# Performance work log

Hardware: AMD Instinct MI355X
Metric: run time of the kernel (lower is better)

Reference implementation:

```python
import jax, jax.numpy as jnp
import numpy as np

D_MODEL = 1024
D_FFN = 4096
NUM_EXPERTS = 8
TOP_K = 2
EPS = 1e-7


def setup_inputs() -> dict:
    key = jax.random.key(0)
    ks = jax.random.split(key, 10)
    B, T = 2, 2048
    s = 0.02
    return {
        "x": jax.random.normal(ks[0], (B, T, D_MODEL), dtype=jnp.float32),
        "padding_mask": jnp.ones((B, T), dtype=bool),
        "rms_w": jnp.ones((D_MODEL,), dtype=jnp.float32),
        "router_w": jax.random.normal(ks[1], (NUM_EXPERTS, D_MODEL), dtype=jnp.float32) * s,
        "router_b": jnp.zeros((NUM_EXPERTS,), dtype=jnp.float32),
        "W1": jax.random.normal(ks[2], (NUM_EXPERTS, D_MODEL, D_FFN), dtype=jnp.float32) * s,
        "b1": jnp.zeros((NUM_EXPERTS, D_FFN), dtype=jnp.float32),
        "W2": jax.random.normal(ks[3], (NUM_EXPERTS, D_FFN, D_MODEL), dtype=jnp.float32) * s,
        "b2": jnp.zeros((NUM_EXPERTS, D_MODEL), dtype=jnp.float32),
        "W3": jax.random.normal(ks[4], (NUM_EXPERTS, D_MODEL, D_FFN), dtype=jnp.float32) * s,
        "b3": jnp.zeros((NUM_EXPERTS, D_FFN), dtype=jnp.float32),
    }


def reference(x, padding_mask, rms_w, router_w, router_b, W1, b1, W2, b2, W3, b3):
    B, T, d = x.shape
    # RMSNorm
    rms = jnp.sqrt(jnp.mean(x * x, axis=-1, keepdims=True) + EPS)
    xn = rms_w * (x / rms)
    xf = xn.reshape(-1, d)  # [N, d]

    # Router: softmax -> top-k -> renormalize
    logits = xf @ router_w.T + router_b            # [N, E]
    probs = jax.nn.softmax(logits, axis=-1)
    topv, topi = jax.lax.top_k(probs, TOP_K)       # [N, K]
    w = topv / jnp.sum(topv, axis=-1, keepdims=True)
    # Dense combine weights per (token, expert): sum of top-k weights routed to e
    combine = jnp.sum(jax.nn.one_hot(topi, NUM_EXPERTS, dtype=xf.dtype) * w[..., None], axis=1)  # [N, E]

    # Loop over experts via scan (one full-token SwiGLU FFN per expert, masked combine)
    def step(acc, params):
        W1e, b1e, W2e, b2e, W3e, b3e, ce = params
        h = jax.nn.silu(xf @ W1e + b1e) * (xf @ W3e + b3e)  # [N, d_ffn]
        y = h @ W2e + b2e                                    # [N, d]
        return acc + ce[:, None] * y, None

    out, _ = jax.lax.scan(step, jnp.zeros_like(xf), (W1, b1, W2, b2, W3, b3, combine.T))
    aux_loss = jnp.asarray(0.0, dtype=x.dtype)  # use_aux_loss only active in training mode
    return out.reshape(B, T, d), aux_loss
```

## Files before the change

### kernel.cpp

```cpp
#include <hip/hip_runtime.h>
#include <stdint.h>


#define NTOK 4096
#define DM   1024
#define DF   4096
#define NE   8
#define BM   128
#define MAX_RB 72
#define SLOT_CAP (MAX_RB * BM)

typedef _Float16 f16;
typedef __attribute__((ext_vector_type(8))) _Float16 f16x8;
typedef __attribute__((ext_vector_type(4))) _Float16 f16x4;
typedef __attribute__((ext_vector_type(4))) float    f32x4;

__device__ __forceinline__ void gl2lds16(const void* g, void* l) {
  __builtin_amdgcn_global_load_lds(
      (const __attribute__((address_space(1))) unsigned int*)g,
      (__attribute__((address_space(3))) unsigned int*)l, 16, 0, 0);
}

__global__ __launch_bounds__(256) void k_rms_router(
    const float* __restrict__ x, const float* __restrict__ rms_w,
    const float* __restrict__ rw, const float* __restrict__ rbias,
    f16* __restrict__ xn, int* __restrict__ topi, float* __restrict__ topw,
    int* __restrict__ counts)
{
  int t = blockIdx.x;
  int tid = threadIdx.x;
  const float* xr = x + (size_t)t * DM;
  f32x4 xv = *(const f32x4*)(xr + tid * 4);
  f32x4 gw = *(const f32x4*)(rms_w + tid * 4);
  f32x4 gv = xv * gw;

  float v[9];
  v[8] = xv[0]*xv[0] + xv[1]*xv[1] + xv[2]*xv[2] + xv[3]*xv[3];
#pragma unroll
  for (int e = 0; e < NE; ++e) {
    f32x4 wv = *(const f32x4*)(rw + e * DM + tid * 4);
    v[e] = gv[0]*wv[0] + gv[1]*wv[1] + gv[2]*wv[2] + gv[3]*wv[3];
  }
#pragma unroll
  for (int off = 32; off; off >>= 1) {
#pragma unroll
    for (int j = 0; j < 9; ++j) v[j] += __shfl_xor(v[j], off);
  }
  __shared__ float red[4][9];
  int wave = tid >> 6, lane = tid & 63;
  if (lane == 0) {
#pragma unroll
    for (int j = 0; j < 9; ++j) red[wave][j] = v[j];
  }
  __syncthreads();
  float tot[9];
#pragma unroll
  for (int j = 0; j < 9; ++j)
    tot[j] = red[0][j] + red[1][j] + red[2][j] + red[3][j];

  float rinv = 1.0f / sqrtf(tot[8] * (1.0f / DM) + 1e-7f);
  float lg[NE];
#pragma unroll
  for (int e = 0; e < NE; ++e) lg[e] = tot[e] * rinv + rbias[e];

  int e1 = 0; float b1v = lg[0];
#pragma unroll
  for (int e = 1; e < NE; ++e) if (lg[e] > b1v) { b1v = lg[e]; e1 = e; }
  int e2 = -1; float b2v = -1e30f;
#pragma unroll
  for (int e = 0; e < NE; ++e) if (e != e1 && lg[e] > b2v) { b2v = lg[e]; e2 = e; }

  float r2 = expf(b2v - b1v);
  float w1 = 1.0f / (1.0f + r2);
  float w2 = r2 * w1;

  if (tid == 0) {
    topi[t * 2 + 0] = e1; topi[t * 2 + 1] = e2;
    topw[t * 2 + 0] = w1; topw[t * 2 + 1] = w2;
    atomicAdd(&counts[e1], 1);
    atomicAdd(&counts[e2], 1);
  }
  f16x4 o;
#pragma unroll
  for (int i = 0; i < 4; ++i) o[i] = (f16)(gv[i] * rinv);
  *(f16x4*)(xn + (size_t)t * DM + tid * 4) = o;
}

__global__ void k_build(const int* __restrict__ counts, int* __restrict__ po,
                        int2* __restrict__ rbtable, int* __restrict__ total_rb)
{
  if (threadIdx.x != 0 || blockIdx.x != 0) return;
  int off = 0, idx = 0;
  for (int e = 0; e < NE; ++e) {
    int c = counts[e];
    po[e] = off;
    int nrb = (c + BM - 1) / BM;
    for (int r = 0; r < nrb; ++r) { rbtable[idx] = make_int2(e, off + r * BM); ++idx; }
    off += nrb * BM;
  }
  *total_rb = idx;
}

__global__ __launch_bounds__(256) void k_assign(
    const int* __restrict__ topi, const float* __restrict__ topw,
    const int* __restrict__ po, int* __restrict__ cursors,
    int* __restrict__ slot_token, float* __restrict__ slot_w,
    int* __restrict__ tok2slot)
{
  int t = blockIdx.x * 256 + threadIdx.x;
  if (t >= NTOK) return;
#pragma unroll
  for (int k = 0; k < 2; ++k) {
    int e = topi[t * 2 + k];
    int pos = atomicAdd(&cursors[e], 1);
    int slot = po[e] + pos;
    slot_token[slot] = t;
    slot_w[slot] = topw[t * 2 + k];
    tok2slot[t * 2 + k] = slot;
  }
}

__global__ __launch_bounds__(256) void k_convw(
    const float* __restrict__ W1, const float* __restrict__ W3,
    f16* __restrict__ w16)
{
  __shared__ f16 T[64][132];
  int g = blockIdx.x;
  int tensor = g >> 12;
  int rem = g & 4095;
  int e = rem >> 9;
  int t = rem & 511;
  const float* W = (tensor == 0) ? W1 : W3;
  int np = t >> 4, kt = t & 15;
  const float* src = W + (size_t)e * DM * DF + (size_t)(kt * 64) * DF + np * 128;

  int tid = threadIdx.x;
  int q = tid & 31, kb = tid >> 5;
#pragma unroll
  for (int i = 0; i < 8; ++i) {
    int k = kb + 8 * i;
    f32x4 v = *(const f32x4*)(src + (size_t)k * DF + q * 4);
    f16x4 h4 = { (f16)v[0], (f16)v[1], (f16)v[2], (f16)v[3] };
    *(f16x4*)(&T[k][q * 4]) = h4;
  }
  __syncthreads();
  int n = tid >> 1;
  f16* dst = w16 + ((size_t)(tensor * NE + e) * 512 + t) * 8192 + n * 64 + (tid & 1) * 32;
#pragma unroll
  for (int qq = 0; qq < 4; ++qq) {
    int cs = (tid & 1) * 4 + qq;
    int cl = cs ^ (n & 7);
    f16x8 o;
#pragma unroll
    for (int j = 0; j < 8; ++j) o[j] = T[cl * 8 + j][n];
    *(f16x8*)(dst + qq * 8) = o;
  }
}

__global__ __launch_bounds__(256, 3) void k_ffn13(
    const f16* __restrict__ xn, const int* __restrict__ slot_token,
    const int2* __restrict__ rbtable, const int* __restrict__ total_rb,
    const f16* __restrict__ w16,
    const float* __restrict__ b1, const float* __restrict__ b3,
    const float* __restrict__ W2, f16* __restrict__ w16_w2,
    f16* __restrict__ h)
{
  __shared__ __align__(16) f16 As[128 * 64];
  __shared__ __align__(16) f16 Bs[2][128 * 64];

  int bid = blockIdx.x;
  int xcd = bid & 7, i = bid >> 3;
  int rbi = (i / 12) * 3 + (i % 3);
  int np  = xcd * 4 + ((i / 3) & 3);
  int tid = threadIdx.x, lane = tid & 63, wave = tid >> 6;

  bool active = (rbi < *total_rb);
  if (active) {
    int2 ent = rbtable[rbi];
    int e = ent.x, row0 = ent.y;
    int n0 = np * 128;

    int wm = wave >> 1, wn = wave & 1;
    const f16* wb1 = w16 + ((size_t)(0 * NE + e) * 512 + np * 16) * 8192;
    const f16* wb3 = w16 + ((size_t)(1 * NE + e) * 512 + np * 16) * 8192;

    int tok[4];
#pragma unroll
    for (int q = 0; q < 4; ++q) {
      int m = q * 32 + wave * 8 + (lane >> 3);
      int tkn = slot_token[row0 + m];
      tok[q] = (tkn < 0) ? 0 : tkn;
    }
    int csx = (((lane & 7) ^ (lane >> 3)) << 3);
    int lin = wave * 512 + lane * 8;

    f32x4 acc1[4][4], acc3[4][4];
    f32x4 z = {0.f, 0.f, 0.f, 0.f};
#pragma unroll
    for (int i2 = 0; i2 < 4; ++i2)
#pragma unroll
      for (int j = 0; j < 4; ++j) { acc1[i2][j] = z; acc3[i2][j] = z; }

    for (int kt = 0; kt < DM / 64; ++kt) {
      int k0 = kt * 64;
      const f16* s1 = wb1 + (size_t)kt * 8192;
      const f16* s3 = wb3 + (size_t)kt * 8192;
#pragma unroll
      for (int q = 0; q < 4; ++q) {
        gl2lds16(xn + (size_t)tok[q] * DM + k0 + csx,
                 (char*)As + q * 4096 + wave * 1024);
        gl2lds16(s1 + q * 2048 + lin, (char*)Bs[0] + q * 4096 + wave * 1024);
        gl2lds16(s3 + q * 2048 + lin, (char*)Bs[1] + q * 4096 + wave * 1024);
      }
      __syncthreads();
#pragma unroll
      for (int kh = 0; kh < 2; ++kh) {
        int kk = kh * 32 + (lane >> 4) * 8;
        f16x8 a[4];
#pragma unroll
        for (int fm = 0; fm < 4; ++fm) {
          int m = wm * 64 + fm * 16 + (lane & 15);
          a[fm] = *(const f16x8*)((char*)As + m * 128 + 2 * (kk ^ ((m & 7) << 3)));
        }
#pragma unroll
        for (int fn = 0; fn < 4; ++fn) {
          int n = wn * 64 + fn * 16 + (lane & 15);
          f16x8 bf1 = *(const f16x8*)((char*)Bs[0] + n * 128 + 2 * (kk ^ ((n & 7) << 3)));
          f16x8 bf3 = *(const f16x8*)((char*)Bs[1] + n * 128 + 2 * (kk ^ ((n & 7) << 3)));
#pragma unroll
          for (int fm = 0; fm < 4; ++fm) {
            acc1[fm][fn] = __builtin_amdgcn_mfma_f32_16x16x32_f16(a[fm], bf1, acc1[fm][fn], 0, 0, 0);
            acc3[fm][fn] = __builtin_amdgcn_mfma_f32_16x16x32_f16(a[fm], bf3, acc3[fm][fn], 0, 0, 0);
          }
        }
      }
      __syncthreads();
    }
#pragma unroll
    for (int fn = 0; fn < 4; ++fn) {
      int nc = n0 + wn * 64 + fn * 16 + (lane & 15);
      float bb1 = b1[e * DF + nc], bb3 = b3[e * DF + nc];
#pragma unroll
      for (int fm = 0; fm < 4; ++fm) {
        int mbase = wm * 64 + fm * 16 + (lane >> 4) * 4;
#pragma unroll
        for (int r = 0; r < 4; ++r) {
          int sl = mbase + r;
          float u1 = acc1[fm][fn][r] + bb1;
          float u3 = acc3[fm][fn][r] + bb3;
          float hv = (u1 / (1.0f + __expf(-u1))) * u3;
          size_t off = (size_t)(row0 + sl) * DF + (nc & ~63)
                     + ((((nc >> 3) & 7) ^ (sl & 7)) << 3) + (nc & 7);
          h[off] = (f16)hv;
        }
      }
    }
  }

  f16 (*T)[132] = (f16(*)[132])(&Bs[0][0]);
  int q = tid & 31, kb = tid >> 5;
  for (int j = 0; j < 2; ++j) {
    int tile = bid * 2 + j;
    if (tile >= NE * 512) break;
    int e2 = tile >> 9, t2 = tile & 511;
    int np2 = t2 >> 6, kt2 = t2 & 63;
    const float* src = W2 + (size_t)e2 * DM * DF + (size_t)(kt2 * 64) * DM + np2 * 128;
    __syncthreads();
#pragma unroll
    for (int i2 = 0; i2 < 8; ++i2) {
      int k = kb + 8 * i2;
      f32x4 v = *(const f32x4*)(src + (size_t)k * DM + q * 4);
      f16x4 h4 = { (f16)v[0], (f16)v[1], (f16)v[2], (f16)v[3] };
      *(f16x4*)(&T[k][q * 4]) = h4;
    }
    __syncthreads();
    int n = tid >> 1;
    f16* dst = w16_w2 + (size_t)(e2 * 512 + t2) * 8192 + n * 64 + (tid & 1) * 32;
#pragma unroll
    for (int qq = 0; qq < 4; ++qq) {
      int cs = (tid & 1) * 4 + qq;
      int cl = cs ^ (n & 7);
      f16x8 o8;
#pragma unroll
      for (int jj = 0; jj < 8; ++jj) o8[jj] = T[cl * 8 + jj][n];
      *(f16x8*)(dst + qq * 8) = o8;
    }
  }
}

__global__ __launch_bounds__(256, 4) void k_ffn2(
    const f16* __restrict__ h,
    const int2* __restrict__ rbtable, const int* __restrict__ total_rb,
    const f16* __restrict__ w16_w2, f16* __restrict__ partial)
{
  __shared__ __align__(16) f16 As[128 * 64];
  __shared__ __align__(16) f16 Bsh[128 * 64];

  int bid = blockIdx.x;
  int xcd = bid & 7, i = bid >> 3;
  int rbi_in  = i % 3;
  int np      = (i / 3) & 7;
  int kc      = (i / 24) & 1;
  int rbi_out = i / 48;
  int rbi = xcd + 8 * (rbi_out * 3 + rbi_in);
  if (rbi >= *total_rb) return;
  int2 ent = rbtable[rbi];
  int e = ent.x, row0 = ent.y;
  int n0 = np * 128;

  int tid = threadIdx.x, lane = tid & 63, wave = tid >> 6;
  int wm = wave >> 1, wn = wave & 1;
  const f16* wb = w16_w2 + ((size_t)e * 512 + np * 64 + kc * 32) * 8192;
  int lin = wave * 512 + lane * 8;

  f32x4 acc[4][4];
  f32x4 z = {0.f, 0.f, 0.f, 0.f};
#pragma unroll
  for (int i2 = 0; i2 < 4; ++i2)
#pragma unroll
    for (int j = 0; j < 4; ++j) acc[i2][j] = z;

  for (int kt = 0; kt < 32; ++kt) {
    const f16* sB = wb + (size_t)kt * 8192;
    int k0 = kc * 2048 + kt * 64;
#pragma unroll
    for (int q = 0; q < 4; ++q) {
      int m = q * 32 + wave * 8 + (lane >> 3);
      gl2lds16(h + (size_t)(row0 + m) * DF + k0 + ((lane & 7) << 3),
               (char*)As + q * 4096 + wave * 1024);
      gl2lds16(sB + q * 2048 + lin, (char*)Bsh + q * 4096 + wave * 1024);
    }
    __syncthreads();
#pragma unroll
    for (int kh = 0; kh < 2; ++kh) {
      int kk = kh * 32 + (lane >> 4) * 8;
      f16x8 a[4];
#pragma unroll
      for (int fm = 0; fm < 4; ++fm) {
        int m = wm * 64 + fm * 16 + (lane & 15);
        a[fm] = *(const f16x8*)((char*)As + m * 128 + 2 * (kk ^ ((m & 7) << 3)));
      }
#pragma unroll
      for (int fn = 0; fn < 4; ++fn) {
        int n = wn * 64 + fn * 16 + (lane & 15);
        f16x8 bf = *(const f16x8*)((char*)Bsh + n * 128 + 2 * (kk ^ ((n & 7) << 3)));
#pragma unroll
        for (int fm = 0; fm < 4; ++fm)
          acc[fm][fn] = __builtin_amdgcn_mfma_f32_16x16x32_f16(a[fm], bf, acc[fm][fn], 0, 0, 0);
      }
    }
    __syncthreads();
  }
#pragma unroll
  for (int fn = 0; fn < 4; ++fn) {
    int nc = n0 + wn * 64 + fn * 16 + (lane & 15);
#pragma unroll
    for (int fm = 0; fm < 4; ++fm) {
      int mbase = wm * 64 + fm * 16 + (lane >> 4) * 4;
#pragma unroll
      for (int r = 0; r < 4; ++r) {
        int slot = row0 + mbase + r;
        partial[((size_t)(kc * SLOT_CAP + slot) << 10) + nc] = (f16)acc[fm][fn][r];
      }
    }
  }
}

__global__ __launch_bounds__(256) void k_combine(
    const f16* __restrict__ partial, const int* __restrict__ tok2slot,
    const int* __restrict__ topi, const float* __restrict__ topw,
    const float* __restrict__ b2, float* __restrict__ out)
{
  int t = blockIdx.x;
  int nc = threadIdx.x * 4;
  int s1 = tok2slot[t * 2], s2 = tok2slot[t * 2 + 1];
  float c1 = topw[t * 2], c2 = topw[t * 2 + 1];
  int e1 = topi[t * 2], e2 = topi[t * 2 + 1];
  float y1[4] = {0.f, 0.f, 0.f, 0.f}, y2[4] = {0.f, 0.f, 0.f, 0.f};
#pragma unroll
  for (int kc = 0; kc < 2; ++kc) {
    f16x4 p1 = *(const f16x4*)(partial + (((size_t)(kc * SLOT_CAP + s1)) << 10) + nc);
    f16x4 p2 = *(const f16x4*)(partial + (((size_t)(kc * SLOT_CAP + s2)) << 10) + nc);
#pragma unroll
    for (int i = 0; i < 4; ++i) { y1[i] += (float)p1[i]; y2[i] += (float)p2[i]; }
  }
  f32x4 bb1 = *(const f32x4*)(b2 + e1 * DM + nc);
  f32x4 bb2 = *(const f32x4*)(b2 + e2 * DM + nc);
  f32x4 o;
#pragma unroll
  for (int i = 0; i < 4; ++i)
    o[i] = c1 * (y1[i] + bb1[i]) + c2 * (y2[i] + bb2[i]);
  *(f32x4*)(out + ((size_t)t << 10) + nc) = o;
}

extern "C" void kernel_launch(void* const* d_in, const int* in_sizes, int n_in,
                              void* d_out, int out_size, void* d_ws, size_t ws_size,
                              hipStream_t stream)
{
  const float* x     = (const float*)d_in[0];
  const float* rms_w = (const float*)d_in[2];
  const float* rw    = (const float*)d_in[3];
  const float* rbias = (const float*)d_in[4];
  const float* W1    = (const float*)d_in[5];
  const float* b1    = (const float*)d_in[6];
  const float* W2    = (const float*)d_in[7];
  const float* b2    = (const float*)d_in[8];
  const float* W3    = (const float*)d_in[9];
  const float* b3    = (const float*)d_in[10];
  float* out = (float*)d_out;

  char* ws = (char*)d_ws;
  size_t o = 0;
  f16* w16 = (f16*)(ws + o); o += (size_t)3 * NE * 512 * 8192 * 2;
  f16* h   = (f16*)(ws + o); o += (size_t)SLOT_CAP * DF * 2;
  f16* xn  = (f16*)(ws + o); o += (size_t)NTOK * DM * 2;
  int*   slot_token = (int*)(ws + o);   o += SLOT_CAP * 4;
  float* slot_w     = (float*)(ws + o); o += SLOT_CAP * 4;
  int*   topi       = (int*)(ws + o);   o += NTOK * 2 * 4;
  float* topw       = (float*)(ws + o); o += NTOK * 2 * 4;
  int*   tok2slot   = (int*)(ws + o);   o += NTOK * 2 * 4;
  int*   counts     = (int*)(ws + o);   o += 64;
  int*   cursors    = (int*)(ws + o);   o += 64;
  int*   po         = (int*)(ws + o);   o += 64;
  int*   total_rb   = (int*)(ws + o);   o += 64;
  int2*  rbtable    = (int2*)(ws + o);  o += MAX_RB * 8;
  (void)ws_size; (void)in_sizes; (void)n_in;

  f16* w16_w2 = w16 + (size_t)2 * NE * 512 * 8192;
  f16* partial = w16;

  size_t covered = (size_t)NTOK * DM;
  if ((size_t)out_size > covered)
    hipMemsetAsync((char*)d_out + covered * 4, 0, ((size_t)out_size - covered) * 4, stream);
  hipMemsetAsync(counts, 0, 128, stream);
  hipMemsetAsync(slot_token, 0xFF, SLOT_CAP * 4, stream);

  k_convw<<<2 * NE * 512, 256, 0, stream>>>(W1, W3, w16);
  k_rms_router<<<NTOK, 256, 0, stream>>>(x, rms_w, rw, rbias, xn, topi, topw, counts);
  k_build<<<1, 64, 0, stream>>>(counts, po, rbtable, total_rb);
  k_assign<<<16, 256, 0, stream>>>(topi, topw, po, cursors, slot_token, slot_w, tok2slot);
  k_ffn13<<<8 * 288, 256, 0, stream>>>(xn, slot_token, rbtable, total_rb,
                                       w16, b1, b3, W2, w16_w2, h);
  k_ffn2<<<8 * 144, 256, 0, stream>>>(h, rbtable, total_rb, w16_w2, partial);
  k_combine<<<NTOK, 256, 0, stream>>>(partial, tok2slot, topi, topw, b2, out);
}
```

Baseline: 520.9 us.

## Merge weight conversion with RMS/router kernel and drop split-K in FFN2

The W1/W3 fp16 conversion kernel and the RMSNorm/router kernel are fused into one launch, with the block index choosing the role, to remove one launch boundary and let the two independent jobs overlap. The down-projection kernel no longer splits K into two halves. Each block now runs the full 4096-long reduction, which halves the grid and removes the second partial buffer read in the combine step. In exchange the FFN2 grid has fewer blocks (576 vs 1152) and may underfill the GPU, and each block's serial work doubles.

```diff
diff --git a/kernel.cpp b/kernel.cpp
--- a/kernel.cpp
+++ b/kernel.cpp
@@ -21,14 +21,52 @@
       (__attribute__((address_space(3))) unsigned int*)l, 16, 0, 0);
 }
 
-__global__ __launch_bounds__(256) void k_rms_router(
+__global__ __launch_bounds__(256) void k_conv_rms(
+    const float* __restrict__ W1, const float* __restrict__ W3,
+    f16* __restrict__ w16,
     const float* __restrict__ x, const float* __restrict__ rms_w,
     const float* __restrict__ rw, const float* __restrict__ rbias,
     f16* __restrict__ xn, int* __restrict__ topi, float* __restrict__ topw,
     int* __restrict__ counts)
 {
-  int t = blockIdx.x;
+  __shared__ f16 T[64][132];
+  __shared__ float red[4][9];
   int tid = threadIdx.x;
+
+  if (blockIdx.x < 2 * NE * 512) {
+    int g = blockIdx.x;
+    int tensor = g >> 12;
+    int rem = g & 4095;
+    int e = rem >> 9;
+    int t = rem & 511;
+    const float* W = (tensor == 0) ? W1 : W3;
+    int np = t >> 4, kt = t & 15;
+    const float* src = W + (size_t)e * DM * DF + (size_t)(kt * 64) * DF + np * 128;
+
+    int q = tid & 31, kb = tid >> 5;
+#pragma unroll
+    for (int i = 0; i < 8; ++i) {
+      int k = kb + 8 * i;
+      f32x4 v = *(const f32x4*)(src + (size_t)k * DF + q * 4);
+      f16x4 h4 = { (f16)v[0], (f16)v[1], (f16)v[2], (f16)v[3] };
+      *(f16x4*)(&T[k][q * 4]) = h4;
+    }
+    __syncthreads();
+    int n = tid >> 1;
+    f16* dst = w16 + ((size_t)(tensor * NE + e) * 512 + t) * 8192 + n * 64 + (tid & 1) * 32;
+#pragma unroll
+    for (int qq = 0; qq < 4; ++qq) {
+      int cs = (tid & 1) * 4 + qq;
+      int cl = cs ^ (n & 7);
+      f16x8 o;
+#pragma unroll
+      for (int j = 0; j < 8; ++j) o[j] = T[cl * 8 + j][n];
+      *(f16x8*)(dst + qq * 8) = o;
+    }
+    return;
+  }
+
+  int t = blockIdx.x - 2 * NE * 512;
   const float* xr = x + (size_t)t * DM;
   f32x4 xv = *(const f32x4*)(xr + tid * 4);
   f32x4 gw = *(const f32x4*)(rms_w + tid * 4);
@@ -46,7 +84,6 @@
 #pragma unroll
     for (int j = 0; j < 9; ++j) v[j] += __shfl_xor(v[j], off);
   }
-  __shared__ float red[4][9];
   int wave = tid >> 6, lane = tid & 63;
   if (lane == 0) {
 #pragma unroll
@@ -117,43 +154,6 @@
     slot_token[slot] = t;
     slot_w[slot] = topw[t * 2 + k];
     tok2slot[t * 2 + k] = slot;
-  }
-}
-
-__global__ __launch_bounds__(256) void k_convw(
-    const float* __restrict__ W1, const float* __restrict__ W3,
-    f16* __restrict__ w16)
-{
-  __shared__ f16 T[64][132];
-  int g = blockIdx.x;
-  int tensor = g >> 12;
-  int rem = g & 4095;
-  int e = rem >> 9;
-  int t = rem & 511;
-  const float* W = (tensor == 0) ? W1 : W3;
-  int np = t >> 4, kt = t & 15;
-  const float* src = W + (size_t)e * DM * DF + (size_t)(kt * 64) * DF + np * 128;
-
-  int tid = threadIdx.x;
-  int q = tid & 31, kb = tid >> 5;
-#pragma unroll
-  for (int i = 0; i < 8; ++i) {
-    int k = kb + 8 * i;
-    f32x4 v = *(const f32x4*)(src + (size_t)k * DF + q * 4);
-    f16x4 h4 = { (f16)v[0], (f16)v[1], (f16)v[2], (f16)v[3] };
-    *(f16x4*)(&T[k][q * 4]) = h4;
-  }
-  __syncthreads();
-  int n = tid >> 1;
-  f16* dst = w16 + ((size_t)(tensor * NE + e) * 512 + t) * 8192 + n * 64 + (tid & 1) * 32;
-#pragma unroll
-  for (int qq = 0; qq < 4; ++qq) {
-    int cs = (tid & 1) * 4 + qq;
-    int cl = cs ^ (n & 7);
-    f16x8 o;
-#pragma unroll
-    for (int j = 0; j < 8; ++j) o[j] = T[cl * 8 + j][n];
-    *(f16x8*)(dst + qq * 8) = o;
   }
 }
 
@@ -299,9 +299,8 @@
   int bid = blockIdx.x;
   int xcd = bid & 7, i = bid >> 3;
   int rbi_in  = i % 3;
-  int np      = (i / 3) & 7;
-  int kc      = (i / 24) & 1;
-  int rbi_out = i / 48;
+  int np      = (i / 3) % 8;
+  int rbi_out = i / 24;
   int rbi = xcd + 8 * (rbi_out * 3 + rbi_in);
   if (rbi >= *total_rb) return;
   int2 ent = rbtable[rbi];
@@ -310,7 +309,7 @@
 
   int tid = threadIdx.x, lane = tid & 63, wave = tid >> 6;
   int wm = wave >> 1, wn = wave & 1;
-  const f16* wb = w16_w2 + ((size_t)e * 512 + np * 64 + kc * 32) * 8192;
+  const f16* wb = w16_w2 + ((size_t)e * 512 + np * 64) * 8192;
   int lin = wave * 512 + lane * 8;
 
   f32x4 acc[4][4];
@@ -320,9 +319,9 @@
 #pragma unroll
     for (int j = 0; j < 4; ++j) acc[i2][j] = z;
 
-  for (int kt = 0; kt < 32; ++kt) {
+  for (int kt = 0; kt < 64; ++kt) {
     const f16* sB = wb + (size_t)kt * 8192;
-    int k0 = kc * 2048 + kt * 64;
+    int k0 = kt * 64;
 #pragma unroll
     for (int q = 0; q < 4; ++q) {
       int m = q * 32 + wave * 8 + (lane >> 3);
@@ -360,7 +359,7 @@
 #pragma unroll
       for (int r = 0; r < 4; ++r) {
         int slot = row0 + mbase + r;
-        partial[((size_t)(kc * SLOT_CAP + slot) << 10) + nc] = (f16)acc[fm][fn][r];
+        partial[((size_t)slot << 10) + nc] = (f16)acc[fm][fn][r];
       }
     }
   }
@@ -376,20 +375,14 @@
   int s1 = tok2slot[t * 2], s2 = tok2slot[t * 2 + 1];
   float c1 = topw[t * 2], c2 = topw[t * 2 + 1];
   int e1 = topi[t * 2], e2 = topi[t * 2 + 1];
-  float y1[4] = {0.f, 0.f, 0.f, 0.f}, y2[4] = {0.f, 0.f, 0.f, 0.f};
-#pragma unroll
-  for (int kc = 0; kc < 2; ++kc) {
-    f16x4 p1 = *(const f16x4*)(partial + (((size_t)(kc * SLOT_CAP + s1)) << 10) + nc);
-    f16x4 p2 = *(const f16x4*)(partial + (((size_t)(kc * SLOT_CAP + s2)) << 10) + nc);
-#pragma unroll
-    for (int i = 0; i < 4; ++i) { y1[i] += (float)p1[i]; y2[i] += (float)p2[i]; }
-  }
+  f16x4 p1 = *(const f16x4*)(partial + ((size_t)s1 << 10) + nc);
+  f16x4 p2 = *(const f16x4*)(partial + ((size_t)s2 << 10) + nc);
   f32x4 bb1 = *(const f32x4*)(b2 + e1 * DM + nc);
   f32x4 bb2 = *(const f32x4*)(b2 + e2 * DM + nc);
   f32x4 o;
 #pragma unroll
   for (int i = 0; i < 4; ++i)
-    o[i] = c1 * (y1[i] + bb1[i]) + c2 * (y2[i] + bb2[i]);
+    o[i] = c1 * ((float)p1[i] + bb1[i]) + c2 * ((float)p2[i] + bb2[i]);
   *(f32x4*)(out + ((size_t)t << 10) + nc) = o;
 }
 
@@ -435,12 +428,12 @@
   hipMemsetAsync(counts, 0, 128, stream);
   hipMemsetAsync(slot_token, 0xFF, SLOT_CAP * 4, stream);
 
-  k_convw<<<2 * NE * 512, 256, 0, stream>>>(W1, W3, w16);
-  k_rms_router<<<NTOK, 256, 0, stream>>>(x, rms_w, rw, rbias, xn, topi, topw, counts);
+  k_conv_rms<<<2 * NE * 512 + NTOK, 256, 0, stream>>>(
+      W1, W3, w16, x, rms_w, rw, rbias, xn, topi, topw, counts);
   k_build<<<1, 64, 0, stream>>>(counts, po, rbtable, total_rb);
   k_assign<<<16, 256, 0, stream>>>(topi, topw, po, cursors, slot_token, slot_w, tok2slot);
   k_ffn13<<<8 * 288, 256, 0, stream>>>(xn, slot_token, rbtable, total_rb,
                                        w16, b1, b3, W2, w16_w2, h);
-  k_ffn2<<<8 * 144, 256, 0, stream>>>(h, rbtable, total_rb, w16_w2, partial);
+  k_ffn2<<<8 * 72, 256, 0, stream>>>(h, rbtable, total_rb, w16_w2, partial);
   k_combine<<<NTOK, 256, 0, stream>>>(partial, tok2slot, topi, topw, b2, out);
 }
```

New measurement: 500.2 us. 4.0% less time.
